# Kernel optimization log

Hardware: AMD Instinct MI355X
Metric: run time of the kernel (lower is better)

Reference implementation:

```python
import jax, jax.numpy as jnp
import numpy as np

D_MODEL = 1024
D_FF = 4096


def _layernorm(x, gamma, beta, eps=1e-5):
    mu = jnp.mean(x, axis=-1, keepdims=True)
    var = jnp.var(x, axis=-1, keepdims=True)
    return (x - mu) * jax.lax.rsqrt(var + eps) * gamma + beta


def setup_inputs() -> dict:
    key = jax.random.key(0)
    ks = jax.random.split(key, 7)
    B, S = 4, 2048
    src = jax.random.normal(ks[0], (B, S, D_MODEL), dtype=jnp.float32)
    gamma1 = jnp.ones((D_MODEL,), jnp.float32)
    beta1 = jnp.zeros((D_MODEL,), jnp.float32)
    gamma2 = jnp.ones((D_MODEL,), jnp.float32)
    beta2 = jnp.zeros((D_MODEL,), jnp.float32)
    w1 = jax.random.normal(ks[1], (D_MODEL, D_FF), jnp.float32) * (1.0 / np.sqrt(D_MODEL))
    b1 = jnp.zeros((D_FF,), jnp.float32)
    w2 = jax.random.normal(ks[2], (D_FF, D_MODEL), jnp.float32) * (1.0 / np.sqrt(D_FF))
    b2 = jnp.zeros((D_MODEL,), jnp.float32)
    return {"src": src, "gamma1": gamma1, "beta1": beta1,
            "gamma2": gamma2, "beta2": beta2,
            "w1": w1, "b1": b1, "w2": w2, "b2": b2}


def reference(src, gamma1, beta1, gamma2, beta2, w1, b1, w2, b2):
    # Pre-LN self-attention (single head, Q=K=V=norm_x, no projections)
    norm_x = _layernorm(src, gamma1, beta1)
    dim_k = norm_x.shape[-1]
    scores = jnp.einsum('bqd,bkd->bqk', norm_x, norm_x) / jnp.sqrt(jnp.float32(dim_k))
    weights = jax.nn.softmax(scores, axis=-1)
    attn = jnp.einsum('bqk,bkd->bqd', weights, norm_x)
    x = src + attn  # dropout p=0 -> identity
    # Pre-LN FFN
    h = _layernorm(x, gamma2, beta2)
    h = jax.nn.gelu(h @ w1 + b1, approximate=False)
    h = h @ w2 + b2
    return h + x
```

## Files before the change

kernel.cpp:

```cpp
#include <hip/hip_runtime.h>
#include <hip/hip_bf16.h>
#include <math.h>

typedef __attribute__((ext_vector_type(8))) short s8vec;
typedef __attribute__((ext_vector_type(16))) float f32x16;
typedef __attribute__((ext_vector_type(4))) unsigned short us4;
typedef __attribute__((ext_vector_type(8))) unsigned short us8;

__device__ __forceinline__ unsigned short f2bf(float f) {
  unsigned u = __float_as_uint(f);
  u = (u + 0x7fffu + ((u >> 16) & 1u)) >> 16;
  return (unsigned short)u;
}
__device__ __forceinline__ float bf2f(unsigned short u) {
  return __uint_as_float(((unsigned)u) << 16);
}

__device__ __forceinline__ float fast_gelu(float t) {
  float t2 = t * t;
  float u = t * (1.59576912f + 0.07135481f * t2);
  float e = __expf(-u);
  return t * __frcp_rn(1.0f + e);
}

__device__ __forceinline__ void async_ld16(const unsigned short* g, unsigned short* l) {
  __builtin_amdgcn_global_load_lds(
      (__attribute__((address_space(1))) void*)g,
      (__attribute__((address_space(3))) void*)l, 16, 0, 0);
}

#define SB0() __builtin_amdgcn_sched_barrier(0)


#define GSTA(j, tk, bofs)                                                   \
  async_ld16(srcA0 + (size_t)(j) * 32 * K + ((size_t)(tk) << 6),            \
             &As[(bofs) + ldsS0 + (j) * 2048])
#define GSTB(j, tk, bofs)                                                   \
  async_ld16(srcB0 + (size_t)(j) * 32 * K + ((size_t)(tk) << 6),            \
             &Bs[(bofs) + ldsS0 + (j) * 2048])

template <int EPI>
__global__ __launch_bounds__(512, 4) void gemm2b(
    const unsigned short* __restrict__ A, const unsigned short* __restrict__ B,
    float* __restrict__ outF, unsigned short* __restrict__ outB,
    const float* __restrict__ bias, const float* __restrict__ res,
    int M, int N, int K,
    long long bA, long long bB, long long bO, long long bR, float scale)
{
  constexpr int TBUF = 128 * 64;
  __shared__ __align__(16) unsigned short As[2 * TBUF];
  __shared__ __align__(16) unsigned short Bs[2 * TBUF];

  (void)M;
  const int tid = threadIdx.x;
  const int w = tid >> 6;
  const int l = tid & 63;

  const unsigned gx = gridDim.x, gy = gridDim.y;
  unsigned lin = blockIdx.x + gx * (blockIdx.y + gy * blockIdx.z);
  const unsigned nwg = gx * gy * gridDim.z;
  lin = (lin & 7u) * (nwg >> 3) + (lin >> 3);
  const unsigned bx = lin & (gx - 1u);
  const unsigned tmp = lin >> __builtin_ctz(gx);
  const unsigned by = tmp & (gy - 1u);
  const unsigned bz = tmp >> __builtin_ctz(gy);

  const int z = (int)bz;
  A += (size_t)z * bA;
  B += (size_t)z * bB;
  const size_t tileM = (size_t)by * 128;
  const size_t tileN = (size_t)bx * 128;

  const int rowbase = (w & 3) * 8 + (w >> 2) * 64;
  const int cS = (l & 7) ^ (l >> 3) ^ (w & 3);
  const unsigned short* srcA0 = A + (tileM + rowbase + (l >> 3)) * (size_t)K + (cS << 3);
  const unsigned short* srcB0 = B + (tileN + rowbase + (l >> 3)) * (size_t)K + (cS << 3);
  const int ldsS0 = rowbase * 64;

  const int wm = w >> 2;
  const int wn = w & 3;
  const int fr = l & 31;
  const int fq = l >> 5;
  const int swz = (l & 7) ^ ((l >> 3) & 3);
  int pc[4];
#pragma unroll
  for (int s = 0; s < 4; ++s) pc[s] = ((((s << 1) + fq) ^ swz) << 3);
  const int aoff0 = (wm * 64 + fr) * 64;
  const int aoff1 = (wm * 64 + 32 + fr) * 64;
  const int boff = (wn * 32 + fr) * 64;

  f32x16 acc[2] = {};
  const int NT = K >> 6;

  GSTB(0, 0, 0); GSTB(1, 0, 0); GSTA(0, 0, 0); GSTA(1, 0, 0);
  GSTB(0, 1, TBUF); GSTB(1, 1, TBUF); GSTA(0, 1, TBUF);
  asm volatile("s_waitcnt vmcnt(3)" ::: "memory");
  __builtin_amdgcn_s_barrier();

  for (int t = 0; t < NT; ++t) {
    const int bf = t & 1;
    const int cb = bf * TBUF, ob = (bf ^ 1) * TBUF;
    const bool g1 = (t + 1 < NT), g2 = (t + 2 < NT);
    s8vec b[4], aA[4], aC[4];

#pragma unroll
    for (int s = 0; s < 4; ++s) {
      b[s]  = *(const s8vec*)&Bs[cb + boff + pc[s]];
      aA[s] = *(const s8vec*)&As[cb + aoff0 + pc[s]];
    }
    SB0();
#pragma unroll
    for (int s = 0; s < 4; ++s)
      aC[s] = *(const s8vec*)&As[cb + aoff1 + pc[s]];
    if (g1) GSTA(1, t + 1, ob);
    SB0();
    asm volatile("s_waitcnt lgkmcnt(4)" ::: "memory");
    SB0();
    __builtin_amdgcn_s_setprio(1);
#pragma unroll
    for (int s = 0; s < 4; ++s)
      acc[0] = __builtin_amdgcn_mfma_f32_32x32x16_bf16(aA[s], b[s], acc[0], 0, 0, 0);
    SB0();
    __builtin_amdgcn_s_setprio(0);
    __builtin_amdgcn_s_barrier();

    if (g2) { GSTB(0, t + 2, cb); GSTB(1, t + 2, cb); GSTA(0, t + 2, cb); }
    SB0();
    asm volatile("s_waitcnt lgkmcnt(0)" ::: "memory");
    SB0();
    __builtin_amdgcn_s_setprio(1);
#pragma unroll
    for (int s = 0; s < 4; ++s)
      acc[1] = __builtin_amdgcn_mfma_f32_32x32x16_bf16(aC[s], b[s], acc[1], 0, 0, 0);
    SB0();
    __builtin_amdgcn_s_setprio(0);
    if (g2) asm volatile("s_waitcnt vmcnt(3)" ::: "memory");
    else    asm volatile("s_waitcnt vmcnt(0)" ::: "memory");
    __builtin_amdgcn_s_barrier();
  }

  float* oF = outF + (size_t)z * bO;
  unsigned short* oB = outB + (size_t)z * bO;
  const float* rs = res + (size_t)z * bR;

  float bc = 0.f;
  if (EPI >= 2) bc = bias[tileN + wn * 32 + fr];

#pragma unroll
  for (int mf = 0; mf < 2; ++mf) {
#pragma unroll
    for (int r = 0; r < 16; ++r) {
      const size_t row = tileM + wm * 64 + (mf << 5) + (r & 3) + ((r >> 2) << 3) + (fq << 2);
      const size_t rb = row * (size_t)N;
      const size_t col = tileN + wn * 32 + fr;
      const float v = acc[mf][r];
      if (EPI == 0) {
        oB[rb + col] = f2bf(v * scale);
      } else if (EPI == 1) {
        oF[rb + col] = v + rs[rb + col];
      } else if (EPI == 2) {
        oB[rb + col] = f2bf(fast_gelu(v + bc));
      } else {
        oF[rb + col] = v + bc + rs[rb + col];
      }
    }
  }
}


#define STA(q, tk, bofs)                                                    \
  async_ld16(srcA0 + (size_t)(q) * 32 * K + ((size_t)(tk) << 6),            \
             &As[(bofs) + ldsA0 + (q) * 2048])
#define STB(j, tk, bofs)                                                    \
  async_ld16(srcB0 + (size_t)(j) * 64 * K + ((size_t)(tk) << 6),            \
             &Bs[(bofs) + ldsB0 + (j) * 4096])

template <int BN, int EPI>
__global__ __launch_bounds__(512, 2) void gemm_nt8(
    const unsigned short* __restrict__ A, const unsigned short* __restrict__ B,
    float* __restrict__ outF, unsigned short* __restrict__ outB,
    const float* __restrict__ bias, const float* __restrict__ res,
    int M, int N, int K,
    long long bA, long long bB, long long bO, long long bR, float scale)
{
  static_assert(BN == 256 || BN == 128, "BN must be 256 or 128");
  constexpr int NB = BN / 64;
  constexpr int NF = BN / 128;
  constexpr int WN = BN / 4;
  constexpr int ABUF = 256 * 64;
  constexpr int BBUF = BN * 64;

  __shared__ __align__(16) unsigned short As[2 * ABUF];
  __shared__ __align__(16) unsigned short Bs[2 * BBUF];

  (void)M;
  const int tid = threadIdx.x;
  const int w = tid >> 6;
  const int l = tid & 63;

  const unsigned gx = gridDim.x, gy = gridDim.y;
  unsigned lin = blockIdx.x + gx * (blockIdx.y + gy * blockIdx.z);
  const unsigned nwg = gx * gy * gridDim.z;
  lin = (lin & 7u) * (nwg >> 3) + (lin >> 3);
  const unsigned bx = lin & (gx - 1u);
  const unsigned tmp = lin >> __builtin_ctz(gx);
  const unsigned by = tmp & (gy - 1u);
  const unsigned bz = tmp >> __builtin_ctz(gy);

  const int z = (int)bz;
  A += (size_t)z * bA;
  B += (size_t)z * bB;
  const size_t tileM = (size_t)by * 256;
  const size_t tileN = (size_t)bx * BN;

  const int sub = w & 3, half = w >> 2;
  const int rA = sub * 8 + half * 128 + (l >> 3);
  const int cA = (l & 7) ^ (rA & 7) ^ ((rA >> 3) & 3);
  const unsigned short* srcA0 = A + (tileM + rA) * (size_t)K + (cA << 3);
  const int ldsA0 = (sub * 8 + half * 128) * 64;

  const int rB = w * 8 + (l >> 3);
  const int cB = (l & 7) ^ (rB & 7) ^ ((rB >> 3) & 3);
  const unsigned short* srcB0 = B + (tileN + rB) * (size_t)K + (cB << 3);
  const int ldsB0 = (w * 8) * 64;

  const int wm = half;
  const int wn = sub;
  const int fr = l & 31;
  const int fq = l >> 5;
  const int swz = (l & 7) ^ ((l >> 3) & 3);
  int pc[4];
#pragma unroll
  for (int s = 0; s < 4; ++s) pc[s] = ((((s << 1) + fq) ^ swz) << 3);
  const int aoff = (wm * 128 + fr) * 64;
  int boff[NF];
#pragma unroll
  for (int nf = 0; nf < NF; ++nf) boff[nf] = (wn * WN + nf * 32 + fr) * 64;

  f32x16 acc[4][NF] = {};
  const int NT = K >> 6;

  STA(0, 0, 0); STA(1, 0, 0); STA(2, 0, 0); STA(3, 0, 0);
#pragma unroll
  for (int j = 0; j < NB; ++j) STB(j, 0, 0);
#pragma unroll
  for (int j = 0; j < NB; ++j) STB(j, 1, BBUF);
  STA(0, 1, ABUF); STA(1, 1, ABUF);
  if constexpr (NB == 4) asm volatile("s_waitcnt vmcnt(6)" ::: "memory");
  else                   asm volatile("s_waitcnt vmcnt(4)" ::: "memory");
  __builtin_amdgcn_s_barrier();

  auto tile = [&](int t, int bf) {
    const int aB = bf * ABUF, bBo = bf * BBUF, oaB = (bf ^ 1) * ABUF;
    const bool g1 = (t + 1 < NT), g2 = (t + 2 < NT);
    s8vec b[NF][4], aA[2][4], aC[2][4];

#pragma unroll
    for (int s = 0; s < 4; ++s) {
#pragma unroll
      for (int nf = 0; nf < NF; ++nf)
        b[nf][s] = *(const s8vec*)&Bs[bBo + boff[nf] + pc[s]];
      aA[0][s] = *(const s8vec*)&As[aB + aoff + 0 * 2048 + pc[s]];
      aA[1][s] = *(const s8vec*)&As[aB + aoff + 1 * 2048 + pc[s]];
    }
    SB0();
#pragma unroll
    for (int s = 0; s < 4; ++s) {
      aC[0][s] = *(const s8vec*)&As[aB + aoff + 2 * 2048 + pc[s]];
      aC[1][s] = *(const s8vec*)&As[aB + aoff + 3 * 2048 + pc[s]];
    }
    if (g1) { STA(2, t + 1, oaB); STA(3, t + 1, oaB); }
    SB0();
    asm volatile("s_waitcnt lgkmcnt(8)" ::: "memory");
    SB0();
    __builtin_amdgcn_s_setprio(1);
#pragma unroll
    for (int s = 0; s < 4; ++s)
#pragma unroll
      for (int i = 0; i < 2; ++i)
#pragma unroll
        for (int nf = 0; nf < NF; ++nf)
          acc[i][nf] = __builtin_amdgcn_mfma_f32_32x32x16_bf16(aA[i][s], b[nf][s], acc[i][nf], 0, 0, 0);
    SB0();
    __builtin_amdgcn_s_setprio(0);
    __builtin_amdgcn_s_barrier();

    if (g2) {
#pragma unroll
      for (int j = 0; j < NB; ++j) STB(j, t + 2, bBo);
      STA(0, t + 2, aB); STA(1, t + 2, aB);
    }
    SB0();
    asm volatile("s_waitcnt lgkmcnt(0)" ::: "memory");
    SB0();
    __builtin_amdgcn_s_setprio(1);
#pragma unroll
    for (int s = 0; s < 4; ++s)
#pragma unroll
      for (int i = 0; i < 2; ++i)
#pragma unroll
        for (int nf = 0; nf < NF; ++nf)
          acc[2 + i][nf] = __builtin_amdgcn_mfma_f32_32x32x16_bf16(aC[i][s], b[nf][s], acc[2 + i][nf], 0, 0, 0);
    SB0();
    __builtin_amdgcn_s_setprio(0);
    if (g2) {
      if constexpr (NB == 4) asm volatile("s_waitcnt vmcnt(6)" ::: "memory");
      else                   asm volatile("s_waitcnt vmcnt(4)" ::: "memory");
    } else {
      asm volatile("s_waitcnt vmcnt(0)" ::: "memory");
    }
    __builtin_amdgcn_s_barrier();
  };

  for (int t = 0; t < NT; t += 2) { tile(t, 0); tile(t + 1, 1); }

  float* oF = outF + (size_t)z * bO;
  unsigned short* oB = outB + (size_t)z * bO;
  const float* rs = res + (size_t)z * bR;

  float bcol[NF];
  if (EPI >= 2) {
#pragma unroll
    for (int nf = 0; nf < NF; ++nf) bcol[nf] = bias[tileN + wn * WN + nf * 32 + fr];
  }

#pragma unroll
  for (int mf = 0; mf < 4; ++mf) {
#pragma unroll
    for (int r = 0; r < 16; ++r) {
      const size_t row = tileM + wm * 128 + (mf << 5) + (r & 3) + ((r >> 2) << 3) + (fq << 2);
      const size_t rb = row * (size_t)N;
#pragma unroll
      for (int nf = 0; nf < NF; ++nf) {
        const size_t col = tileN + wn * WN + (nf << 5) + fr;
        const float v = acc[mf][nf][r];
        if (EPI == 0) {
          oB[rb + col] = f2bf(v * scale);
        } else if (EPI == 1) {
          oF[rb + col] = v + rs[rb + col];
        } else if (EPI == 2) {
          oB[rb + col] = f2bf(fast_gelu(v + bcol[nf]));
        } else {
          oF[rb + col] = v + bcol[nf] + rs[rb + col];
        }
      }
    }
  }
}

__global__ __launch_bounds__(256) void ln_row(
    const float* __restrict__ x, const float* __restrict__ gamma,
    const float* __restrict__ beta, unsigned short* __restrict__ out)
{
  const int row = blockIdx.x;
  const float4* xr = (const float4*)(x + (size_t)row * 1024);
  const int tid = threadIdx.x;
  float4 v = xr[tid];
  float s = v.x + v.y + v.z + v.w;
  float q = v.x * v.x + v.y * v.y + v.z * v.z + v.w * v.w;
#pragma unroll
  for (int off = 32; off > 0; off >>= 1) {
    s += __shfl_down(s, off);
    q += __shfl_down(q, off);
  }
  __shared__ float rs_[4], rq_[4];
  const int w = tid >> 6, l = tid & 63;
  if (l == 0) { rs_[w] = s; rq_[w] = q; }
  __syncthreads();
  s = rs_[0] + rs_[1] + rs_[2] + rs_[3];
  q = rq_[0] + rq_[1] + rq_[2] + rq_[3];
  const float mu = s * (1.0f / 1024.0f);
  const float var = q * (1.0f / 1024.0f) - mu * mu;
  const float rstd = rsqrtf(var + 1e-5f);
  const float4 g = ((const float4*)gamma)[tid];
  const float4 b = ((const float4*)beta)[tid];
  us4 o;
  o.x = f2bf((v.x - mu) * rstd * g.x + b.x);
  o.y = f2bf((v.y - mu) * rstd * g.y + b.y);
  o.z = f2bf((v.z - mu) * rstd * g.z + b.z);
  o.w = f2bf((v.w - mu) * rstd * g.w + b.w);
  ((us4*)(out + (size_t)row * 1024))[tid] = o;
}

__global__ __launch_bounds__(256) void softmax_row(
    const unsigned short* __restrict__ sc, unsigned short* __restrict__ pr)
{
  const int row = blockIdx.x;
  const s8vec* s8 = (const s8vec*)(sc + (size_t)row * 2048);
  const int tid = threadIdx.x;
  s8vec a = s8[tid];
  float x[8];
#pragma unroll
  for (int i = 0; i < 8; ++i) x[i] = bf2f((unsigned short)a[i]);
  float mx = x[0];
#pragma unroll
  for (int i = 1; i < 8; ++i) mx = fmaxf(mx, x[i]);
#pragma unroll
  for (int off = 32; off > 0; off >>= 1) mx = fmaxf(mx, __shfl_down(mx, off));
  __shared__ float red[4];
  const int w = tid >> 6, l = tid & 63;
  if (l == 0) red[w] = mx;
  __syncthreads();
  mx = fmaxf(fmaxf(red[0], red[1]), fmaxf(red[2], red[3]));
  __syncthreads();
  float e[8], s = 0.f;
#pragma unroll
  for (int i = 0; i < 8; ++i) { e[i] = __expf(x[i] - mx); s += e[i]; }
#pragma unroll
  for (int off = 32; off > 0; off >>= 1) s += __shfl_down(s, off);
  if (l == 0) red[w] = s;
  __syncthreads();
  s = red[0] + red[1] + red[2] + red[3];
  const float inv = 1.0f / s;
  s8vec o;
#pragma unroll
  for (int i = 0; i < 8; ++i) o[i] = (short)f2bf(e[i] * inv);
  ((s8vec*)(pr + (size_t)row * 2048))[tid] = o;
}

__global__ __launch_bounds__(256) void tconv_f32(
    const float* __restrict__ in, unsigned short* __restrict__ out, int R, int C)
{
  __shared__ float tile[64][65];
  const int tid = threadIdx.x;
  const int c0 = blockIdx.x * 64, r0 = blockIdx.y * 64;
#pragma unroll
  for (int k2 = 0; k2 < 4; ++k2) {
    const int idx = tid + k2 * 256;
    const int row = idx >> 4, c4 = (idx & 15) << 2;
    const float4 v = *(const float4*)&in[(size_t)(r0 + row) * C + c0 + c4];
    tile[row][c4] = v.x; tile[row][c4 + 1] = v.y;
    tile[row][c4 + 2] = v.z; tile[row][c4 + 3] = v.w;
  }
  __syncthreads();
#pragma unroll
  for (int k2 = 0; k2 < 4; ++k2) {
    const int idx = tid + k2 * 256;
    const int cc = idx >> 4, r4 = (idx & 15) << 2;
    us4 o;
#pragma unroll
    for (int j = 0; j < 4; ++j) o[j] = f2bf(tile[r4 + j][cc]);
    *(us4*)&out[(size_t)(c0 + cc) * R + r0 + r4] = o;
  }
}

__global__ __launch_bounds__(256) void tconv_bf16(
    const unsigned short* __restrict__ in, unsigned short* __restrict__ out,
    int R, int C, long long bIn, long long bOut)
{
  __shared__ unsigned short tile[64][66];
  const int tid = threadIdx.x;
  const int z = blockIdx.z;
  in += (size_t)z * bIn;
  out += (size_t)z * bOut;
  const int c0 = blockIdx.x * 64, r0 = blockIdx.y * 64;
#pragma unroll
  for (int k2 = 0; k2 < 2; ++k2) {
    const int idx = tid + k2 * 256;
    const int row = idx >> 3, c8 = (idx & 7) << 3;
    const us8 v = *(const us8*)&in[(size_t)(r0 + row) * C + c0 + c8];
#pragma unroll
    for (int j = 0; j < 8; ++j) tile[row][c8 + j] = v[j];
  }
  __syncthreads();
#pragma unroll
  for (int k2 = 0; k2 < 4; ++k2) {
    const int idx = tid + k2 * 256;
    const int cc = idx >> 4, r4 = (idx & 15) << 2;
    us4 o;
#pragma unroll
    for (int j = 0; j < 4; ++j) o[j] = tile[r4 + j][cc];
    *(us4*)&out[(size_t)(c0 + cc) * R + r0 + r4] = o;
  }
}

extern "C" void kernel_launch(void* const* d_in, const int* in_sizes, int n_in,
                              void* d_out, int out_size, void* d_ws, size_t ws_size,
                              hipStream_t stream)
{
  (void)in_sizes; (void)n_in; (void)out_size; (void)ws_size;
  const float* src = (const float*)d_in[0];
  const float* g1  = (const float*)d_in[1];
  const float* be1 = (const float*)d_in[2];
  const float* g2  = (const float*)d_in[3];
  const float* be2 = (const float*)d_in[4];
  const float* w1  = (const float*)d_in[5];
  const float* b1  = (const float*)d_in[6];
  const float* w2  = (const float*)d_in[7];
  const float* b2  = (const float*)d_in[8];
  float* out = (float*)d_out;

  char* ws = (char*)d_ws;
  const size_t SZ_NORMX  = (size_t)8192 * 1024 * 2;
  const size_t SZ_SCORES = (size_t)4 * 2048 * 2048 * 4;
  const size_t SZ_PROBS  = (size_t)4 * 2048 * 2048 * 2;
  const size_t SZ_X      = (size_t)8192 * 1024 * 4;
  const size_t SZ_W1T    = (size_t)1024 * 4096 * 2;

  unsigned short* normx  = (unsigned short*)(ws);
  unsigned short* normxT = (unsigned short*)(ws + SZ_NORMX);
  unsigned short* scores = (unsigned short*)(ws + 2 * SZ_NORMX);
  unsigned short* probs  = (unsigned short*)(ws + 2 * SZ_NORMX + SZ_SCORES);
  float*          xbuf   = (float*)(ws + 2 * SZ_NORMX + SZ_SCORES + SZ_PROBS);
  unsigned short* w1t    = (unsigned short*)(ws + 2 * SZ_NORMX + SZ_SCORES + SZ_PROBS + SZ_X);
  unsigned short* w2t    = (unsigned short*)(ws + 2 * SZ_NORMX + SZ_SCORES + SZ_PROBS + SZ_X + SZ_W1T);
  unsigned short* normx2 = normx;
  unsigned short* hbuf   = scores;

  tconv_f32<<<dim3(64, 16), 256, 0, stream>>>(w1, w1t, 1024, 4096);
  tconv_f32<<<dim3(16, 64), 256, 0, stream>>>(w2, w2t, 4096, 1024);

  ln_row<<<8192, 256, 0, stream>>>(src, g1, be1, normx);
  tconv_bf16<<<dim3(16, 32, 4), 256, 0, stream>>>(
      normx, normxT, 2048, 1024, (long long)2048 * 1024, (long long)1024 * 2048);

  gemm2b<0><<<dim3(16, 16, 4), 512, 0, stream>>>(
      normx, normx, nullptr, scores, nullptr, nullptr,
      2048, 2048, 1024,
      (long long)2048 * 1024, (long long)2048 * 1024, (long long)2048 * 2048, 0, 0.03125f);

  softmax_row<<<8192, 256, 0, stream>>>(scores, probs);

  gemm_nt8<128, 1><<<dim3(8, 8, 4), 512, 0, stream>>>(
      probs, normxT, xbuf, nullptr, nullptr, src,
      2048, 1024, 2048,
      (long long)2048 * 2048, (long long)1024 * 2048, (long long)2048 * 1024,
      (long long)2048 * 1024, 1.0f);

  ln_row<<<8192, 256, 0, stream>>>(xbuf, g2, be2, normx2);

  gemm2b<2><<<dim3(32, 64, 1), 512, 0, stream>>>(
      normx2, w1t, nullptr, hbuf, b1, nullptr,
      8192, 4096, 1024, 0, 0, 0, 0, 1.0f);

  gemm_nt8<128, 3><<<dim3(8, 32, 1), 512, 0, stream>>>(
      hbuf, w2t, out, nullptr, b2, xbuf,
      8192, 1024, 4096, 0, 0, 0, 0, 1.0f);
}
```

Baseline: 415.6 us.

## Run first FFN GEMM in FP8 and use 256-wide tiles for scores GEMM

```diff
diff --git a/kernel.cpp b/kernel.cpp
--- a/kernel.cpp
+++ b/kernel.cpp
@@ -6,6 +6,7 @@
 typedef __attribute__((ext_vector_type(16))) float f32x16;
 typedef __attribute__((ext_vector_type(4))) unsigned short us4;
 typedef __attribute__((ext_vector_type(8))) unsigned short us8;
+typedef long long i64frag;
 
 __device__ __forceinline__ unsigned short f2bf(float f) {
   unsigned u = __float_as_uint(f);
@@ -14,6 +15,24 @@
 }
 __device__ __forceinline__ float bf2f(unsigned short u) {
   return __uint_as_float(((unsigned)u) << 16);
+}
+
+__device__ __forceinline__ unsigned char f2e4m3(float f) {
+  unsigned u = __float_as_uint(f);
+  unsigned s = (u >> 24) & 0x80u;
+  float a = __uint_as_float(u & 0x7FFFFFFFu);
+  a = fminf(a, 448.0f);
+  unsigned char m;
+  if (a < 0.015625f) {
+    m = (unsigned char)__float2int_rn(a * 512.0f);
+  } else {
+    unsigned x = __float_as_uint(a);
+    x += 0x0007FFFFu + ((x >> 20) & 1u);
+    int e = (int)(x >> 23) - 120;
+    if (e >= 16) m = 0x7E;
+    else m = (unsigned char)((e << 3) | ((x >> 20) & 7u));
+  }
+  return (unsigned char)(s | m);
 }
 
 __device__ __forceinline__ float fast_gelu(float t) {
@@ -28,144 +47,13 @@
       (__attribute__((address_space(1))) void*)g,
       (__attribute__((address_space(3))) void*)l, 16, 0, 0);
 }
+__device__ __forceinline__ void async_ld16b(const unsigned char* g, unsigned char* l) {
+  __builtin_amdgcn_global_load_lds(
+      (__attribute__((address_space(1))) void*)g,
+      (__attribute__((address_space(3))) void*)l, 16, 0, 0);
+}
 
 #define SB0() __builtin_amdgcn_sched_barrier(0)
-
-
-#define GSTA(j, tk, bofs)                                                   \
-  async_ld16(srcA0 + (size_t)(j) * 32 * K + ((size_t)(tk) << 6),            \
-             &As[(bofs) + ldsS0 + (j) * 2048])
-#define GSTB(j, tk, bofs)                                                   \
-  async_ld16(srcB0 + (size_t)(j) * 32 * K + ((size_t)(tk) << 6),            \
-             &Bs[(bofs) + ldsS0 + (j) * 2048])
-
-template <int EPI>
-__global__ __launch_bounds__(512, 4) void gemm2b(
-    const unsigned short* __restrict__ A, const unsigned short* __restrict__ B,
-    float* __restrict__ outF, unsigned short* __restrict__ outB,
-    const float* __restrict__ bias, const float* __restrict__ res,
-    int M, int N, int K,
-    long long bA, long long bB, long long bO, long long bR, float scale)
-{
-  constexpr int TBUF = 128 * 64;
-  __shared__ __align__(16) unsigned short As[2 * TBUF];
-  __shared__ __align__(16) unsigned short Bs[2 * TBUF];
-
-  (void)M;
-  const int tid = threadIdx.x;
-  const int w = tid >> 6;
-  const int l = tid & 63;
-
-  const unsigned gx = gridDim.x, gy = gridDim.y;
-  unsigned lin = blockIdx.x + gx * (blockIdx.y + gy * blockIdx.z);
-  const unsigned nwg = gx * gy * gridDim.z;
-  lin = (lin & 7u) * (nwg >> 3) + (lin >> 3);
-  const unsigned bx = lin & (gx - 1u);
-  const unsigned tmp = lin >> __builtin_ctz(gx);
-  const unsigned by = tmp & (gy - 1u);
-  const unsigned bz = tmp >> __builtin_ctz(gy);
-
-  const int z = (int)bz;
-  A += (size_t)z * bA;
-  B += (size_t)z * bB;
-  const size_t tileM = (size_t)by * 128;
-  const size_t tileN = (size_t)bx * 128;
-
-  const int rowbase = (w & 3) * 8 + (w >> 2) * 64;
-  const int cS = (l & 7) ^ (l >> 3) ^ (w & 3);
-  const unsigned short* srcA0 = A + (tileM + rowbase + (l >> 3)) * (size_t)K + (cS << 3);
-  const unsigned short* srcB0 = B + (tileN + rowbase + (l >> 3)) * (size_t)K + (cS << 3);
-  const int ldsS0 = rowbase * 64;
-
-  const int wm = w >> 2;
-  const int wn = w & 3;
-  const int fr = l & 31;
-  const int fq = l >> 5;
-  const int swz = (l & 7) ^ ((l >> 3) & 3);
-  int pc[4];
-#pragma unroll
-  for (int s = 0; s < 4; ++s) pc[s] = ((((s << 1) + fq) ^ swz) << 3);
-  const int aoff0 = (wm * 64 + fr) * 64;
-  const int aoff1 = (wm * 64 + 32 + fr) * 64;
-  const int boff = (wn * 32 + fr) * 64;
-
-  f32x16 acc[2] = {};
-  const int NT = K >> 6;
-
-  GSTB(0, 0, 0); GSTB(1, 0, 0); GSTA(0, 0, 0); GSTA(1, 0, 0);
-  GSTB(0, 1, TBUF); GSTB(1, 1, TBUF); GSTA(0, 1, TBUF);
-  asm volatile("s_waitcnt vmcnt(3)" ::: "memory");
-  __builtin_amdgcn_s_barrier();
-
-  for (int t = 0; t < NT; ++t) {
-    const int bf = t & 1;
-    const int cb = bf * TBUF, ob = (bf ^ 1) * TBUF;
-    const bool g1 = (t + 1 < NT), g2 = (t + 2 < NT);
-    s8vec b[4], aA[4], aC[4];
-
-#pragma unroll
-    for (int s = 0; s < 4; ++s) {
-      b[s]  = *(const s8vec*)&Bs[cb + boff + pc[s]];
-      aA[s] = *(const s8vec*)&As[cb + aoff0 + pc[s]];
-    }
-    SB0();
-#pragma unroll
-    for (int s = 0; s < 4; ++s)
-      aC[s] = *(const s8vec*)&As[cb + aoff1 + pc[s]];
-    if (g1) GSTA(1, t + 1, ob);
-    SB0();
-    asm volatile("s_waitcnt lgkmcnt(4)" ::: "memory");
-    SB0();
-    __builtin_amdgcn_s_setprio(1);
-#pragma unroll
-    for (int s = 0; s < 4; ++s)
-      acc[0] = __builtin_amdgcn_mfma_f32_32x32x16_bf16(aA[s], b[s], acc[0], 0, 0, 0);
-    SB0();
-    __builtin_amdgcn_s_setprio(0);
-    __builtin_amdgcn_s_barrier();
-
-    if (g2) { GSTB(0, t + 2, cb); GSTB(1, t + 2, cb); GSTA(0, t + 2, cb); }
-    SB0();
-    asm volatile("s_waitcnt lgkmcnt(0)" ::: "memory");
-    SB0();
-    __builtin_amdgcn_s_setprio(1);
-#pragma unroll
-    for (int s = 0; s < 4; ++s)
-      acc[1] = __builtin_amdgcn_mfma_f32_32x32x16_bf16(aC[s], b[s], acc[1], 0, 0, 0);
-    SB0();
-    __builtin_amdgcn_s_setprio(0);
-    if (g2) asm volatile("s_waitcnt vmcnt(3)" ::: "memory");
-    else    asm volatile("s_waitcnt vmcnt(0)" ::: "memory");
-    __builtin_amdgcn_s_barrier();
-  }
-
-  float* oF = outF + (size_t)z * bO;
-  unsigned short* oB = outB + (size_t)z * bO;
-  const float* rs = res + (size_t)z * bR;
-
-  float bc = 0.f;
-  if (EPI >= 2) bc = bias[tileN + wn * 32 + fr];
-
-#pragma unroll
-  for (int mf = 0; mf < 2; ++mf) {
-#pragma unroll
-    for (int r = 0; r < 16; ++r) {
-      const size_t row = tileM + wm * 64 + (mf << 5) + (r & 3) + ((r >> 2) << 3) + (fq << 2);
-      const size_t rb = row * (size_t)N;
-      const size_t col = tileN + wn * 32 + fr;
-      const float v = acc[mf][r];
-      if (EPI == 0) {
-        oB[rb + col] = f2bf(v * scale);
-      } else if (EPI == 1) {
-        oF[rb + col] = v + rs[rb + col];
-      } else if (EPI == 2) {
-        oB[rb + col] = f2bf(fast_gelu(v + bc));
-      } else {
-        oF[rb + col] = v + bc + rs[rb + col];
-      }
-    }
-  }
-}
 
 
 #define STA(q, tk, bofs)                                                    \
@@ -348,6 +236,153 @@
   }
 }
 
+
+#define F8STA(q, tk, bofs)                                                  \
+  async_ld16b(srcA0 + (size_t)(q) * 32 * K + (size_t)(tk) * 128,            \
+              &As8[(bofs) + ldsA0 + (q) * 4096])
+#define F8STB(j, tk, bofs)                                                  \
+  async_ld16b(srcB0 + (size_t)(j) * 64 * K + (size_t)(tk) * 128,            \
+              &Bs8[(bofs) + ldsB0 + (j) * 8192])
+
+__global__ __launch_bounds__(512, 2) void gemm_fp8(
+    const unsigned char* __restrict__ A, const unsigned char* __restrict__ B,
+    unsigned short* __restrict__ outB, const float* __restrict__ bias,
+    int N, int K, float scale)
+{
+  constexpr int ABUF8 = 256 * 128;
+  constexpr int BBUF8 = 256 * 128;
+  __shared__ __align__(16) unsigned char As8[2 * ABUF8];
+  __shared__ __align__(16) unsigned char Bs8[2 * BBUF8];
+
+  const int tid = threadIdx.x;
+  const int w = tid >> 6;
+  const int l = tid & 63;
+
+  const unsigned gx = gridDim.x, gy = gridDim.y;
+  unsigned lin = blockIdx.x + gx * blockIdx.y;
+  const unsigned nwg = gx * gy;
+  lin = (lin & 7u) * (nwg >> 3) + (lin >> 3);
+  const unsigned bx = lin & (gx - 1u);
+  const unsigned by = lin >> __builtin_ctz(gx);
+
+  const size_t tileM = (size_t)by * 256;
+  const size_t tileN = (size_t)bx * 256;
+
+  const int sub = w & 3, half = w >> 2;
+  const int rA = sub * 8 + half * 128 + (l >> 3);
+  const int cA = (l & 7) ^ (rA & 7) ^ ((rA >> 3) & 3);
+  const unsigned char* srcA0 = A + (tileM + rA) * (size_t)K + (cA << 4);
+  const int ldsA0 = (sub * 8 + half * 128) * 128;
+
+  const int rB = w * 8 + (l >> 3);
+  const int cB = (l & 7) ^ (rB & 7) ^ ((rB >> 3) & 3);
+  const unsigned char* srcB0 = B + (tileN + rB) * (size_t)K + (cB << 4);
+  const int ldsB0 = (w * 8) * 128;
+
+  const int wm = half, wn = sub;
+  const int fr = l & 31;
+  const int fq = l >> 5;
+  const int swz = (l & 7) ^ ((l >> 3) & 3);
+  int pr[8];
+#pragma unroll
+  for (int p = 0; p < 8; ++p) pr[p] = ((p ^ swz) << 4) + (fq << 3);
+  const int aoffB = (wm * 128 + fr) * 128;
+  int boffB[2];
+#pragma unroll
+  for (int nf = 0; nf < 2; ++nf) boffB[nf] = (wn * 64 + nf * 32 + fr) * 128;
+
+  f32x16 acc[4][2] = {};
+  const int NT = K >> 7;
+
+  F8STA(0, 0, 0); F8STA(1, 0, 0); F8STA(2, 0, 0); F8STA(3, 0, 0);
+#pragma unroll
+  for (int j = 0; j < 4; ++j) F8STB(j, 0, 0);
+#pragma unroll
+  for (int j = 0; j < 4; ++j) F8STB(j, 1, BBUF8);
+  F8STA(0, 1, ABUF8); F8STA(1, 1, ABUF8);
+  asm volatile("s_waitcnt vmcnt(6)" ::: "memory");
+  __builtin_amdgcn_s_barrier();
+
+  auto tile = [&](int t, int bf) {
+    const int aB = bf * ABUF8, bBo = bf * BBUF8, oaB = (bf ^ 1) * ABUF8;
+    const bool g1 = (t + 1 < NT), g2 = (t + 2 < NT);
+    i64frag b[2][8], aA[2][8], aC[2][8];
+
+#pragma unroll
+    for (int s = 0; s < 8; ++s) {
+      b[0][s]  = *(const i64frag*)&Bs8[bBo + boffB[0] + pr[s]];
+      b[1][s]  = *(const i64frag*)&Bs8[bBo + boffB[1] + pr[s]];
+      aA[0][s] = *(const i64frag*)&As8[aB + aoffB + 0 * 4096 + pr[s]];
+      aA[1][s] = *(const i64frag*)&As8[aB + aoffB + 1 * 4096 + pr[s]];
+    }
+    SB0();
+#pragma unroll
+    for (int s = 0; s < 8; ++s) {
+      aC[0][s] = *(const i64frag*)&As8[aB + aoffB + 2 * 4096 + pr[s]];
+      aC[1][s] = *(const i64frag*)&As8[aB + aoffB + 3 * 4096 + pr[s]];
+    }
+    if (g1) { F8STA(2, t + 1, oaB); F8STA(3, t + 1, oaB); }
+    SB0();
+    asm volatile("s_waitcnt lgkmcnt(12)" ::: "memory");
+    SB0();
+    __builtin_amdgcn_s_setprio(1);
+#pragma unroll
+    for (int s = 0; s < 8; ++s)
+#pragma unroll
+      for (int i = 0; i < 2; ++i)
+#pragma unroll
+        for (int nf = 0; nf < 2; ++nf)
+          acc[i][nf] = __builtin_amdgcn_mfma_f32_32x32x16_fp8_fp8(
+              aA[i][s], b[nf][s], acc[i][nf], 0, 0, 0);
+    SB0();
+    __builtin_amdgcn_s_setprio(0);
+    __builtin_amdgcn_s_barrier();
+
+    if (g2) {
+#pragma unroll
+      for (int j = 0; j < 4; ++j) F8STB(j, t + 2, bBo);
+      F8STA(0, t + 2, aB); F8STA(1, t + 2, aB);
+    }
+    SB0();
+    asm volatile("s_waitcnt lgkmcnt(0)" ::: "memory");
+    SB0();
+    __builtin_amdgcn_s_setprio(1);
+#pragma unroll
+    for (int s = 0; s < 8; ++s)
+#pragma unroll
+      for (int i = 0; i < 2; ++i)
+#pragma unroll
+        for (int nf = 0; nf < 2; ++nf)
+          acc[2 + i][nf] = __builtin_amdgcn_mfma_f32_32x32x16_fp8_fp8(
+              aC[i][s], b[nf][s], acc[2 + i][nf], 0, 0, 0);
+    SB0();
+    __builtin_amdgcn_s_setprio(0);
+    if (g2) asm volatile("s_waitcnt vmcnt(6)" ::: "memory");
+    else    asm volatile("s_waitcnt vmcnt(0)" ::: "memory");
+    __builtin_amdgcn_s_barrier();
+  };
+
+  for (int t = 0; t < NT; t += 2) { tile(t, 0); tile(t + 1, 1); }
+
+  float bcol[2];
+#pragma unroll
+  for (int nf = 0; nf < 2; ++nf) bcol[nf] = bias[tileN + wn * 64 + nf * 32 + fr];
+
+#pragma unroll
+  for (int mf = 0; mf < 4; ++mf) {
+#pragma unroll
+    for (int r = 0; r < 16; ++r) {
+      const size_t row = tileM + wm * 128 + (mf << 5) + (r & 3) + ((r >> 2) << 3) + (fq << 2);
+      const size_t rb = row * (size_t)N;
+#pragma unroll
+      for (int nf = 0; nf < 2; ++nf) {
+        const size_t col = tileN + wn * 64 + (nf << 5) + fr;
+        outB[rb + col] = f2bf(fast_gelu(acc[mf][nf][r] * scale + bcol[nf]));
+      }
+    }
+  }
+}
+
 __global__ __launch_bounds__(256) void ln_row(
     const float* __restrict__ x, const float* __restrict__ gamma,
     const float* __restrict__ beta, unsigned short* __restrict__ out)
@@ -382,6 +417,39 @@
   ((us4*)(out + (size_t)row * 1024))[tid] = o;
 }
 
+__global__ __launch_bounds__(256) void ln_row_fp8(
+    const float* __restrict__ x, const float* __restrict__ gamma,
+    const float* __restrict__ beta, unsigned char* __restrict__ out)
+{
+  const int row = blockIdx.x;
+  const float4* xr = (const float4*)(x + (size_t)row * 1024);
+  const int tid = threadIdx.x;
+  float4 v = xr[tid];
+  float s = v.x + v.y + v.z + v.w;
+  float q = v.x * v.x + v.y * v.y + v.z * v.z + v.w * v.w;
+#pragma unroll
+  for (int off = 32; off > 0; off >>= 1) {
+    s += __shfl_down(s, off);
+    q += __shfl_down(q, off);
+  }
+  __shared__ float rs_[4], rq_[4];
+  const int w = tid >> 6, l = tid & 63;
+  if (l == 0) { rs_[w] = s; rq_[w] = q; }
+  __syncthreads();
+  s = rs_[0] + rs_[1] + rs_[2] + rs_[3];
+  q = rq_[0] + rq_[1] + rq_[2] + rq_[3];
+  const float mu = s * (1.0f / 1024.0f);
+  const float var = q * (1.0f / 1024.0f) - mu * mu;
+  const float rstd = rsqrtf(var + 1e-5f);
+  const float4 g = ((const float4*)gamma)[tid];
+  const float4 b = ((const float4*)beta)[tid];
+  unsigned pack =  (unsigned)f2e4m3((v.x - mu) * rstd * g.x + b.x)
+                | ((unsigned)f2e4m3((v.y - mu) * rstd * g.y + b.y) << 8)
+                | ((unsigned)f2e4m3((v.z - mu) * rstd * g.z + b.z) << 16)
+                | ((unsigned)f2e4m3((v.w - mu) * rstd * g.w + b.w) << 24);
+  ((unsigned*)(out + (size_t)row * 1024))[tid] = pack;
+}
+
 __global__ __launch_bounds__(256) void softmax_row(
     const unsigned short* __restrict__ sc, unsigned short* __restrict__ pr)
 {
@@ -441,6 +509,34 @@
 #pragma unroll
     for (int j = 0; j < 4; ++j) o[j] = f2bf(tile[r4 + j][cc]);
     *(us4*)&out[(size_t)(c0 + cc) * R + r0 + r4] = o;
+  }
+}
+
+__global__ __launch_bounds__(256) void tconv_f32_fp8(
+    const float* __restrict__ in, unsigned char* __restrict__ out,
+    int R, int C, float SC)
+{
+  __shared__ float tile[64][65];
+  const int tid = threadIdx.x;
+  const int c0 = blockIdx.x * 64, r0 = blockIdx.y * 64;
+#pragma unroll
+  for (int k2 = 0; k2 < 4; ++k2) {
+    const int idx = tid + k2 * 256;
+    const int row = idx >> 4, c4 = (idx & 15) << 2;
+    const float4 v = *(const float4*)&in[(size_t)(r0 + row) * C + c0 + c4];
+    tile[row][c4] = v.x; tile[row][c4 + 1] = v.y;
+    tile[row][c4 + 2] = v.z; tile[row][c4 + 3] = v.w;
+  }
+  __syncthreads();
+#pragma unroll
+  for (int k2 = 0; k2 < 4; ++k2) {
+    const int idx = tid + k2 * 256;
+    const int cc = idx >> 4, r4 = (idx & 15) << 2;
+    unsigned pack =  (unsigned)f2e4m3(tile[r4 + 0][cc] * SC)
+                  | ((unsigned)f2e4m3(tile[r4 + 1][cc] * SC) << 8)
+                  | ((unsigned)f2e4m3(tile[r4 + 2][cc] * SC) << 16)
+                  | ((unsigned)f2e4m3(tile[r4 + 3][cc] * SC) << 24);
+    *(unsigned*)&out[(size_t)(c0 + cc) * R + r0 + r4] = pack;
   }
 }
 
@@ -504,17 +600,18 @@
   float*          xbuf   = (float*)(ws + 2 * SZ_NORMX + SZ_SCORES + SZ_PROBS);
   unsigned short* w1t    = (unsigned short*)(ws + 2 * SZ_NORMX + SZ_SCORES + SZ_PROBS + SZ_X);
   unsigned short* w2t    = (unsigned short*)(ws + 2 * SZ_NORMX + SZ_SCORES + SZ_PROBS + SZ_X + SZ_W1T);
-  unsigned short* normx2 = normx;
-  unsigned short* hbuf   = scores;
-
-  tconv_f32<<<dim3(64, 16), 256, 0, stream>>>(w1, w1t, 1024, 4096);
+  unsigned char*  normx28 = (unsigned char*)normx;
+  unsigned char*  w1t8    = (unsigned char*)w1t;
+  unsigned short* hbuf    = scores;
+
+  tconv_f32_fp8<<<dim3(64, 16), 256, 0, stream>>>(w1, w1t8, 1024, 4096, 16.0f);
   tconv_f32<<<dim3(16, 64), 256, 0, stream>>>(w2, w2t, 4096, 1024);
 
   ln_row<<<8192, 256, 0, stream>>>(src, g1, be1, normx);
   tconv_bf16<<<dim3(16, 32, 4), 256, 0, stream>>>(
       normx, normxT, 2048, 1024, (long long)2048 * 1024, (long long)1024 * 2048);
 
-  gemm2b<0><<<dim3(16, 16, 4), 512, 0, stream>>>(
+  gemm_nt8<256, 0><<<dim3(8, 8, 4), 512, 0, stream>>>(
       normx, normx, nullptr, scores, nullptr, nullptr,
       2048, 2048, 1024,
       (long long)2048 * 1024, (long long)2048 * 1024, (long long)2048 * 2048, 0, 0.03125f);
@@ -527,11 +624,10 @@
       (long long)2048 * 2048, (long long)1024 * 2048, (long long)2048 * 1024,
       (long long)2048 * 1024, 1.0f);
 
-  ln_row<<<8192, 256, 0, stream>>>(xbuf, g2, be2, normx2);
-
-  gemm2b<2><<<dim3(32, 64, 1), 512, 0, stream>>>(
-      normx2, w1t, nullptr, hbuf, b1, nullptr,
-      8192, 4096, 1024, 0, 0, 0, 0, 1.0f);
+  ln_row_fp8<<<8192, 256, 0, stream>>>(xbuf, g2, be2, normx28);
+
+  gemm_fp8<<<dim3(16, 32), 512, 0, stream>>>(
+      normx28, w1t8, hbuf, b1, 4096, 1024, 0.0625f);
 
   gemm_nt8<128, 3><<<dim3(8, 32, 1), 512, 0, stream>>>(
       hbuf, w2t, out, nullptr, b2, xbuf,
```

Result: faster. 397.2 us (-4.4%).
